# Kernel tuning notes

Hardware: AMD Instinct MI355X
Metric: run time of the kernel (lower is better)

## Reference

```python
import jax, jax.numpy as jnp
import numpy as np

N_NODES = 50000
N_EDGES = 600000
F_IN = 128   # nfeature
H = 128      # nhidden (must equal nfeature due to original code's gcn2 init)
C = 10       # nclass


def setup_inputs() -> dict:
    key = jax.random.key(0)
    ks = jax.random.split(key, 8)
    row = jax.random.randint(ks[0], (N_EDGES,), 0, N_NODES)
    col = jax.random.randint(ks[1], (N_EDGES,), 0, N_NODES)
    label = jax.random.randint(ks[2], (N_EDGES,), 0, C)
    features = jax.random.normal(ks[3], (N_NODES, F_IN), dtype=jnp.float32)
    s1 = 1.0 / np.sqrt(F_IN)
    W1 = jax.random.uniform(ks[4], (H, F_IN), jnp.float32, -s1, s1)
    b1 = jnp.zeros((H,), jnp.float32)
    s2 = 1.0 / np.sqrt(H)
    W2 = jax.random.uniform(ks[5], (H, H), jnp.float32, -s2, s2)
    b2 = jnp.zeros((H,), jnp.float32)
    s3 = 1.0 / np.sqrt(2 * H)
    Wfc = jax.random.uniform(ks[6], (C, 2 * H), jnp.float32, -s3, s3)
    bfc = jnp.zeros((C,), jnp.float32)
    return {"features": features, "W1": W1, "b1": b1, "W2": W2, "b2": b2,
            "Wfc": Wfc, "bfc": bfc, "row": row, "col": col, "label": label}


def gcn_conv(x, row, col, W, b):
    # GCNConv: add self loops, linear, then deg-normalized scatter-add.
    n = x.shape[0]
    sl = jnp.arange(n, dtype=row.dtype)
    r = jnp.concatenate([row, sl])  # source / j index (PyG edge_index[0])
    c = jnp.concatenate([col, sl])  # target / aggregation index (edge_index[1])
    h = x @ W.T + b  # [N, H]
    # degree computed over row of self-loop-augmented edge_index (>=1 always)
    deg = jax.ops.segment_sum(jnp.ones(r.shape, h.dtype), r, num_segments=n)
    dinv = deg ** -0.5
    norm = dinv[r] * dinv[c]  # [E+N]
    msg = norm[:, None] * h[r]  # gather + scale, [E+N, H]
    return jax.ops.segment_sum(msg, c, num_segments=n)  # scatter-add, [N, H]


def reference(features, W1, b1, W2, b2, Wfc, bfc, row, col, label):
    h1 = gcn_conv(features, row, col, W1, b1)  # [N, H]
    h2 = gcn_conv(h1, row, col, W2, b2)        # [N, H]
    # take_logits: index_select per edge endpoint, concat on feature dim
    x = jnp.concatenate([h2[row], h2[col]], axis=1)  # [E, 2H]
    logits = x @ Wfc.T + bfc  # [E, C]
    logp = jax.nn.log_softmax(logits, axis=-1)
    loss = -jnp.mean(jnp.take_along_axis(logp, label[:, None], axis=1))
    return loss, logits
```

## Files before the change

kernel.cpp:

```cpp
#include <hip/hip_runtime.h>
#include <hip/hip_bf16.h>
#include <math.h>

#define NND 50000
#define NE  600000
#define HD  128
#define NC  10
#define CAP 64
#define NCH 64
#define ECHUNK 9375
#define HBIN8 25000
#define SCB 128
#define HISTB 256
#define PREPB 1040
#define GEMMB 782
#define LOSSB 2344

typedef unsigned short ushort_t;
typedef unsigned char uchar_t;
typedef __attribute__((ext_vector_type(8))) short short8;
typedef __attribute__((ext_vector_type(4))) float f32x4;

__device__ __forceinline__ float bf2f(unsigned short u) {
  return __uint_as_float(((unsigned int)u) << 16);
}
__device__ __forceinline__ unsigned short f2bf(float f) {
  __hip_bfloat16 h = __float2bfloat16(f);
  return *(unsigned short*)&h;
}

__device__ __forceinline__ short8 f2bf8(const float* __restrict__ p) {
  float4 x0 = *(const float4*)p;
  float4 x1 = *(const float4*)(p + 4);
  short8 v;
  v[0] = (short)f2bf(x0.x); v[1] = (short)f2bf(x0.y);
  v[2] = (short)f2bf(x0.z); v[3] = (short)f2bf(x0.w);
  v[4] = (short)f2bf(x1.x); v[5] = (short)f2bf(x1.y);
  v[6] = (short)f2bf(x1.z); v[7] = (short)f2bf(x1.w);
  return v;
}

__global__ __launch_bounds__(256) void k_prep(const int* __restrict__ row,
                                              const int* __restrict__ col,
                                              uchar_t* __restrict__ partC,
                                              uchar_t* __restrict__ partR,
                                              const float* __restrict__ W1,
                                              const float* __restrict__ W2,
                                              const float* __restrict__ Wfc,
                                              const float* __restrict__ b1,
                                              const float* __restrict__ b2,
                                              float* __restrict__ M,
                                              float* __restrict__ uv) {
  __shared__ unsigned int h32[HBIN8 / 4];
  int bb = blockIdx.x, tid = threadIdx.x;
  if (bb < HISTB) {
    const int* src = (bb < SCB) ? col : row;
    uchar_t* dst = (bb < SCB) ? partC : partR;
    int hb = bb & (SCB - 1);
    int cb = hb & 63, half = hb >> 6;
    int binbase = half * HBIN8;
    for (int i = tid; i < HBIN8 / 4; i += 256) h32[i] = 0;
    __syncthreads();
    int e0 = cb * ECHUNK;
    for (int e = e0 + tid; e < e0 + ECHUNK; e += 256) {
      int r = src[e] - binbase;
      if (r >= 0 && r < HBIN8)
        atomicAdd(&h32[r >> 2], 1u << ((r & 3) * 8));
    }
    __syncthreads();
    unsigned int* d32 = (unsigned int*)(dst + (size_t)hb * HBIN8);
    for (int i = tid; i < HBIN8 / 4; i += 256) d32[i] = h32[i];
  } else {
    int wid = (bb - HISTB) * 4 + (tid >> 6);
    int lane = tid & 63;
    int c5 = wid / 130, jj = wid - c5 * 130;
    if (c5 >= 32) return;
    int grp = c5 >> 4, n = c5 & 15;
    bool valid = (n < NC);
    const float* wrow = &Wfc[(valid ? n : 0) * 256 + grp * 128];
    int k0 = lane, k1 = lane + 64;
    float v0 = 0.f, v1 = 0.f;
    for (int m = 0; m < 128; m++) {
      float wm = wrow[m];
      v0 += wm * W2[m * HD + k0];
      v1 += wm * W2[m * HD + k1];
    }
    float t;
    if (jj < 128)       t = v0 * W1[k0 * HD + jj] + v1 * W1[k1 * HD + jj];
    else if (jj == 128) t = v0 * b1[k0] + v1 * b1[k1];
    else                t = wrow[k0] * b2[k0] + wrow[k1] * b2[k1];
    if (!valid) t = 0.f;
    #pragma unroll
    for (int off = 32; off > 0; off >>= 1) t += __shfl_xor(t, off, 64);
    if (lane == 0) {
      if (jj < 128) M[(grp * 16 + n) * HD + jj] = t;
      else if (valid && jj == 128) uv[grp * 10 + n] = t;
      else if (valid) uv[20 + grp * 10 + n] = t;
    }
  }
}

__global__ __launch_bounds__(256) void k_off(const uchar_t* __restrict__ partC,
                                             const uchar_t* __restrict__ partR,
                                             uchar_t* __restrict__ off8,
                                             int* __restrict__ pos,
                                             float* __restrict__ dinv,
                                             float* __restrict__ out) {
  int n = blockIdx.x * 256 + threadIdx.x;
  if (n == 0) out[0] = 0.f;
  if (n >= NND) return;
  int half = (n >= HBIN8) ? 1 : 0;
  int local = n - half * HBIN8;
  int run = 0;
  #pragma unroll 8
  for (int cb = 0; cb < NCH; cb++) {
    int v = partC[(size_t)(half * NCH + cb) * HBIN8 + local];
    off8[(size_t)cb * NND + n] = (uchar_t)run;
    run += v;
  }
  pos[n] = run;
  int rs = 0;
  #pragma unroll 8
  for (int cb = 0; cb < NCH; cb++) rs += partR[(size_t)(half * NCH + cb) * HBIN8 + local];
  dinv[n] = rsqrtf(1.0f + (float)rs);
}

__global__ __launch_bounds__(256) void k_front(const int* __restrict__ row,
                                               const int* __restrict__ col,
                                               const uchar_t* __restrict__ off8,
                                               ushort_t* __restrict__ srcs,
                                               const float* __restrict__ features,
                                               const float* __restrict__ M,
                                               ushort_t* __restrict__ T0) {
  __shared__ unsigned int h32[HBIN8 / 4];
  int tid = threadIdx.x, bb = blockIdx.x;
  if (bb < SCB) {
    int cb = bb & 63, half = bb >> 6;
    int binbase = half * HBIN8;
    for (int i = tid; i < HBIN8 / 4; i += 256) h32[i] = 0;
    __syncthreads();
    int e0 = cb * ECHUNK;
    const uchar_t* offc = &off8[(size_t)cb * NND];
    for (int e = e0 + tid; e < e0 + ECHUNK; e += 256) {
      int c = col[e];
      int r = c - binbase;
      if (r >= 0 && r < HBIN8) {
        unsigned int old = atomicAdd(&h32[r >> 2], 1u << ((r & 3) * 8));
        int loc = (old >> ((r & 3) * 8)) & 0xff;
        int p = offc[c] + loc;
        if (p < CAP) srcs[(size_t)c * CAP + p] = (ushort_t)row[e];
      }
    }
  } else {
    int bid = bb - SCB;
    int w = tid >> 6, lane = tid & 63;
    int m = lane & 15, q = lane >> 4;
    short8 B[8];
    #pragma unroll
    for (int g = 0; g < 8; g++) {
      int grp = g >> 2, t = g & 3;
      B[g] = f2bf8(&M[(grp * 16 + m) * HD + t * 32 + q * 8]);
    }
    int rowbase = bid * 64 + w * 16;
    int rm = rowbase + m; if (rm >= NND) rm = NND - 1;
    short8 a[4];
    #pragma unroll
    for (int t = 0; t < 4; t++)
      a[t] = f2bf8(&features[(long)rm * HD + t * 32 + q * 8]);
    f32x4 accL = {0.f, 0.f, 0.f, 0.f}, accR = {0.f, 0.f, 0.f, 0.f};
    #pragma unroll
    for (int t = 0; t < 4; t++) {
      accL = __builtin_amdgcn_mfma_f32_16x16x32_bf16(a[t], B[t],     accL, 0, 0, 0);
      accR = __builtin_amdgcn_mfma_f32_16x16x32_bf16(a[t], B[4 + t], accR, 0, 0, 0);
    }
    if (m < 12) {
      #pragma unroll
      for (int reg = 0; reg < 4; reg++) {
        int r = rowbase + q * 4 + reg;
        if (r < NND) {
          float vL = (m < 10) ? accL[reg] : ((m == 10) ? 1.0f : 0.0f);
          float vR = (m < 10) ? accR[reg] : 0.0f;
          T0[(long)r * 24 + m]      = f2bf(vL);
          T0[(long)r * 24 + 12 + m] = f2bf(vR);
        }
      }
    }
  }
}

template <bool FINAL>
__global__ __launch_bounds__(256) void k_aggrn(const ushort_t* __restrict__ Q,
                                               const ushort_t* __restrict__ srcs,
                                               const int* __restrict__ pos,
                                               const float* __restrict__ dinv,
                                               ushort_t* __restrict__ T1,
                                               float* __restrict__ Pr,
                                               float* __restrict__ Pc,
                                               const float* __restrict__ uv) {
  int g = threadIdx.x >> 5, lane = threadIdx.x & 31;
  int half = lane >> 4;
  int f = lane & 15;
  int node = blockIdx.x * 8 + g;
  if (node >= NND) return;
  float di = dinv[node];
  bool act = (f < 12);
  unsigned int qv = act ? *(const unsigned int*)&Q[(long)node * 24 + 2 * f] : 0u;
  float sw = (half == 0) ? di * di : 0.f;
  float a0 = sw * bf2f((ushort_t)(qv & 0xffff));
  float a1 = sw * bf2f((ushort_t)(qv >> 16));
  int cnt = pos[node]; if (cnt > CAP) cnt = CAP;
  const ushort_t* nb = &srcs[(long)node * CAP];
  for (int base = 0; base < cnt; base += 32) {
    int m2 = cnt - base; if (m2 > 32) m2 = 32;
    int sl = 0; float wl = 0.f;
    if (lane < m2) { sl = (int)nb[base + lane]; wl = di * dinv[sl]; }
    int iters = (m2 + 1) >> 1;
    int u = 0;
    for (; u + 1 < iters; u += 2) {
      int t0 = 2 * u + half, t1 = t0 + 2;
      int s0 = __shfl(sl, t0 & 31, 32); float w0 = __shfl(wl, t0 & 31, 32);
      int s1 = __shfl(sl, t1 & 31, 32); float w1 = __shfl(wl, t1 & 31, 32);
      unsigned int h0 = act ? *(const unsigned int*)&Q[(long)s0 * 24 + 2 * f] : 0u;
      unsigned int h1 = act ? *(const unsigned int*)&Q[(long)s1 * 24 + 2 * f] : 0u;
      a0 += w0 * bf2f((ushort_t)(h0 & 0xffff));
      a1 += w0 * bf2f((ushort_t)(h0 >> 16));
      a0 += w1 * bf2f((ushort_t)(h1 & 0xffff));
      a1 += w1 * bf2f((ushort_t)(h1 >> 16));
    }
    if (u < iters) {
      int t = 2 * u + half;
      int s = __shfl(sl, t & 31, 32); float wv = __shfl(wl, t & 31, 32);
      unsigned int hs = act ? *(const unsigned int*)&Q[(long)s * 24 + 2 * f] : 0u;
      a0 += wv * bf2f((ushort_t)(hs & 0xffff));
      a1 += wv * bf2f((ushort_t)(hs >> 16));
    }
  }
  a0 += __shfl(a0, f + 16, 32);
  a1 += __shfl(a1, f + 16, 32);
  if (FINAL) {
    float s_i = __shfl(bf2f((ushort_t)(qv & 0xffff)), 5, 32);
    float z2  = __shfl(a0, 5, 32);
    if (half == 0) {
      if (f < 5) {
        int cc = 2 * f;
        float2 v;
        v.x = a0 + z2 * uv[cc]     + s_i * uv[20 + cc];
        v.y = a1 + z2 * uv[cc + 1] + s_i * uv[20 + cc + 1];
        *(float2*)&Pr[(long)node * 12 + cc] = v;
      } else if (f >= 6 && f < 11) {
        int cc = 2 * f - 12;
        float2 v;
        v.x = a0 + z2 * uv[10 + cc]     + s_i * uv[30 + cc];
        v.y = a1 + z2 * uv[10 + cc + 1] + s_i * uv[30 + cc + 1];
        *(float2*)&Pc[(long)node * 12 + cc] = v;
      }
    }
  } else {
    if (half == 0 && act) {
      unsigned int o = ((unsigned int)f2bf(a1) << 16) | (unsigned int)f2bf(a0);
      *(unsigned int*)&T1[(long)node * 24 + 2 * f] = o;
    }
  }
}

__global__ __launch_bounds__(256) void k_edge(const float* __restrict__ Pr,
                                              const float* __restrict__ Pc,
                                              const int* __restrict__ row,
                                              const int* __restrict__ col,
                                              const int* __restrict__ label,
                                              const float* __restrict__ bfc,
                                              float* __restrict__ logits,
                                              float* __restrict__ out) {
  __shared__ __align__(16) float S[2560];
  __shared__ float Ls[4];
  int tid = threadIdx.x;
  long e0 = (long)blockIdx.x * 256;
  int e = (int)e0 + tid;
  float lp = 0.f;
  if (e < NE) {
    int r = row[e], c = col[e];
    const float* pr = &Pr[(long)r * 12];
    const float* pc = &Pc[(long)c * 12];
    float4 r0 = *(const float4*)&pr[0];
    float4 r1 = *(const float4*)&pr[4];
    float4 r2 = *(const float4*)&pr[8];
    float4 c0 = *(const float4*)&pc[0];
    float4 c1 = *(const float4*)&pc[4];
    float4 c2 = *(const float4*)&pc[8];
    float p[NC];
    p[0] = r0.x + c0.x + bfc[0]; p[1] = r0.y + c0.y + bfc[1];
    p[2] = r0.z + c0.z + bfc[2]; p[3] = r0.w + c0.w + bfc[3];
    p[4] = r1.x + c1.x + bfc[4]; p[5] = r1.y + c1.y + bfc[5];
    p[6] = r1.z + c1.z + bfc[6]; p[7] = r1.w + c1.w + bfc[7];
    p[8] = r2.x + c2.x + bfc[8]; p[9] = r2.y + c2.y + bfc[9];
    #pragma unroll
    for (int cc = 0; cc < NC; cc++) S[tid * 10 + cc] = p[cc];
    float mx = p[0];
    #pragma unroll
    for (int cc = 1; cc < NC; cc++) mx = fmaxf(mx, p[cc]);
    float se = 0.f;
    #pragma unroll
    for (int cc = 0; cc < NC; cc++) se += __expf(p[cc] - mx);
    int lb = label[e];
    float plb = p[0];
    #pragma unroll
    for (int cc = 1; cc < NC; cc++) plb = (cc == lb) ? p[cc] : plb;
    lp = plb - mx - __logf(se);
  }
  __syncthreads();
  int ve = NE - (int)e0; if (ve > 256) ve = 256;
  int limF4 = ve * 10 / 4;
  float4* dst = (float4*)&logits[e0 * 10];
  const float4* src4 = (const float4*)S;
  for (int i = tid; i < limF4; i += 256) dst[i] = src4[i];
  #pragma unroll
  for (int off = 32; off > 0; off >>= 1) lp += __shfl_xor(lp, off, 64);
  if ((tid & 63) == 0) Ls[tid >> 6] = lp;
  __syncthreads();
  if (tid == 0)
    atomicAdd(out, -(Ls[0] + Ls[1] + Ls[2] + Ls[3]) / (float)NE);
}

extern "C" void kernel_launch(void* const* d_in, const int* in_sizes, int n_in,
                              void* d_out, int out_size, void* d_ws, size_t ws_size,
                              hipStream_t stream) {
  const float* features = (const float*)d_in[0];
  const float* W1  = (const float*)d_in[1];
  const float* b1  = (const float*)d_in[2];
  const float* W2  = (const float*)d_in[3];
  const float* b2  = (const float*)d_in[4];
  const float* Wfc = (const float*)d_in[5];
  const float* bfc = (const float*)d_in[6];
  const int* row   = (const int*)d_in[7];
  const int* col   = (const int*)d_in[8];
  const int* label = (const int*)d_in[9];
  float* out = (float*)d_out;

  float* ws = (float*)d_ws;
  size_t o = 0;
  int* pos = (int*)(ws + o);            o += 50048;
  float* dinv = ws + o;                 o += 50048;
  ushort_t* srcs = (ushort_t*)(ws + o); o += (size_t)NND * CAP / 2;
  uchar_t* partC = (uchar_t*)(ws + o);  o += SCB * HBIN8 / 4;
  uchar_t* partR = (uchar_t*)(ws + o);  o += SCB * HBIN8 / 4;
  uchar_t* off8  = (uchar_t*)(ws + o);  o += NCH * NND / 4;
  float* Pr = ws + o;                   o += 600000;
  float* Pc = ws + o;                   o += 600000;
  float* uv = ws + o;                   o += 64;
  float* M  = ws + o;                   o += 4096;
  ushort_t* T0 = (ushort_t*)(ws + o);   o += 600000;
  ushort_t* T1 = (ushort_t*)(ws + o);   o += 600000;

  k_prep<<<HISTB + PREPB, 256, 0, stream>>>(row, col, partC, partR,
                                            W1, W2, Wfc, b1, b2, M, uv);
  k_off<<<196, 256, 0, stream>>>(partC, partR, off8, pos, dinv, out);
  k_front<<<SCB + GEMMB, 256, 0, stream>>>(row, col, off8, srcs, features, M, T0);
  k_aggrn<false><<<6250, 256, 0, stream>>>(T0, srcs, pos, dinv, T1, nullptr, nullptr, uv);
  k_aggrn<true><<<6250, 256, 0, stream>>>(T1, srcs, pos, dinv, nullptr, Pr, Pc, uv);
  k_edge<<<LOSSB, 256, 0, stream>>>(Pr, Pc, row, col, label, bfc, out + 1, out);
}
```

Before: 219.6 us.

## Fuse offset computation into histogram kernel via global atomics, drop k_off

Removes the separate offset/degree kernel. Histogram blocks now atomically add their per-chunk bin counts into global pos/deg arrays and store the returned base as the 8-bit offset. The Wfc·W2·W1 precompute is restructured to one block per output row using shared memory, with fewer blocks. Degree normalization is computed on the fly with rsqrt in the aggregation kernels, and a memset is added to zero the counters. This saves one launch and the partial-histogram round trip, but offsets now depend on atomic ordering across chunks rather than chunk order, and many global atomics are added.

Result: slower. 267.1 us (+21.6%).

```diff
diff --git a/kernel.cpp b/kernel.cpp
--- a/kernel.cpp
+++ b/kernel.cpp
@@ -12,7 +12,7 @@
 #define HBIN8 25000
 #define SCB 128
 #define HISTB 256
-#define PREPB 1040
+#define COLB 32
 #define GEMMB 782
 #define LOSSB 2344
 
@@ -42,20 +42,22 @@
 
 __global__ __launch_bounds__(256) void k_prep(const int* __restrict__ row,
                                               const int* __restrict__ col,
-                                              uchar_t* __restrict__ partC,
-                                              uchar_t* __restrict__ partR,
+                                              int* __restrict__ pos,
+                                              int* __restrict__ deg,
+                                              uchar_t* __restrict__ off8,
                                               const float* __restrict__ W1,
                                               const float* __restrict__ W2,
                                               const float* __restrict__ Wfc,
                                               const float* __restrict__ b1,
                                               const float* __restrict__ b2,
                                               float* __restrict__ M,
-                                              float* __restrict__ uv) {
-  __shared__ unsigned int h32[HBIN8 / 4];
+                                              float* __restrict__ uv,
+                                              float* __restrict__ out) {
   int bb = blockIdx.x, tid = threadIdx.x;
   if (bb < HISTB) {
-    const int* src = (bb < SCB) ? col : row;
-    uchar_t* dst = (bb < SCB) ? partC : partR;
+    __shared__ unsigned int h32[HBIN8 / 4];
+    bool isCol = (bb < SCB);
+    const int* src = isCol ? col : row;
     int hb = bb & (SCB - 1);
     int cb = hb & 63, half = hb >> 6;
     int binbase = half * HBIN8;
@@ -68,61 +70,59 @@
         atomicAdd(&h32[r >> 2], 1u << ((r & 3) * 8));
     }
     __syncthreads();
-    unsigned int* d32 = (unsigned int*)(dst + (size_t)hb * HBIN8);
-    for (int i = tid; i < HBIN8 / 4; i += 256) d32[i] = h32[i];
+    if (isCol) {
+      unsigned int* d32 = (unsigned int*)(off8 + (size_t)cb * NND + binbase);
+      int* pb = pos + binbase;
+      for (int i = tid; i < HBIN8 / 4; i += 256) {
+        unsigned int cv = h32[i], ov = 0;
+        #pragma unroll
+        for (int j = 0; j < 4; j++) {
+          int cnt = (cv >> (8 * j)) & 0xff;
+          if (cnt) {
+            int b = atomicAdd(&pb[4 * i + j], cnt);
+            ov |= ((unsigned int)(b & 0xff)) << (8 * j);
+          }
+        }
+        d32[i] = ov;
+      }
+    } else {
+      int* pb = deg + binbase;
+      for (int i = tid; i < HBIN8 / 4; i += 256) {
+        unsigned int cv = h32[i];
+        #pragma unroll
+        for (int j = 0; j < 4; j++) {
+          int cnt = (cv >> (8 * j)) & 0xff;
+          if (cnt) atomicAdd(&pb[4 * i + j], cnt);
+        }
+      }
+    }
   } else {
-    int wid = (bb - HISTB) * 4 + (tid >> 6);
-    int lane = tid & 63;
-    int c5 = wid / 130, jj = wid - c5 * 130;
-    if (c5 >= 32) return;
+    __shared__ float V[128];
+    int c5 = bb - HISTB;
+    if (c5 == 0 && tid == 0) out[0] = 0.f;
     int grp = c5 >> 4, n = c5 & 15;
     bool valid = (n < NC);
     const float* wrow = &Wfc[(valid ? n : 0) * 256 + grp * 128];
-    int k0 = lane, k1 = lane + 64;
-    float v0 = 0.f, v1 = 0.f;
-    for (int m = 0; m < 128; m++) {
-      float wm = wrow[m];
-      v0 += wm * W2[m * HD + k0];
-      v1 += wm * W2[m * HD + k1];
-    }
-    float t;
-    if (jj < 128)       t = v0 * W1[k0 * HD + jj] + v1 * W1[k1 * HD + jj];
-    else if (jj == 128) t = v0 * b1[k0] + v1 * b1[k1];
-    else                t = wrow[k0] * b2[k0] + wrow[k1] * b2[k1];
-    if (!valid) t = 0.f;
-    #pragma unroll
-    for (int off = 32; off > 0; off >>= 1) t += __shfl_xor(t, off, 64);
-    if (lane == 0) {
-      if (jj < 128) M[(grp * 16 + n) * HD + jj] = t;
-      else if (valid && jj == 128) uv[grp * 10 + n] = t;
-      else if (valid) uv[20 + grp * 10 + n] = t;
-    }
-  }
-}
-
-__global__ __launch_bounds__(256) void k_off(const uchar_t* __restrict__ partC,
-                                             const uchar_t* __restrict__ partR,
-                                             uchar_t* __restrict__ off8,
-                                             int* __restrict__ pos,
-                                             float* __restrict__ dinv,
-                                             float* __restrict__ out) {
-  int n = blockIdx.x * 256 + threadIdx.x;
-  if (n == 0) out[0] = 0.f;
-  if (n >= NND) return;
-  int half = (n >= HBIN8) ? 1 : 0;
-  int local = n - half * HBIN8;
-  int run = 0;
-  #pragma unroll 8
-  for (int cb = 0; cb < NCH; cb++) {
-    int v = partC[(size_t)(half * NCH + cb) * HBIN8 + local];
-    off8[(size_t)cb * NND + n] = (uchar_t)run;
-    run += v;
-  }
-  pos[n] = run;
-  int rs = 0;
-  #pragma unroll 8
-  for (int cb = 0; cb < NCH; cb++) rs += partR[(size_t)(half * NCH + cb) * HBIN8 + local];
-  dinv[n] = rsqrtf(1.0f + (float)rs);
+    if (tid < 128) {
+      float s = 0.f;
+      for (int m = 0; m < 128; m++) s += wrow[m] * W2[m * HD + tid];
+      V[tid] = s;
+    }
+    __syncthreads();
+    if (tid < 128) {
+      float t = 0.f;
+      for (int k = 0; k < 128; k++) t += V[k] * W1[k * HD + tid];
+      M[(grp * 16 + n) * HD + tid] = valid ? t : 0.f;
+    } else if (tid == 128 && valid) {
+      float t = 0.f;
+      for (int k = 0; k < 128; k++) t += V[k] * b1[k];
+      uv[grp * 10 + n] = t;
+    } else if (tid == 129 && valid) {
+      float t = 0.f;
+      for (int k = 0; k < 128; k++) t += wrow[k] * b2[k];
+      uv[20 + grp * 10 + n] = t;
+    }
+  }
 }
 
 __global__ __launch_bounds__(256) void k_front(const int* __restrict__ row,
@@ -192,7 +192,7 @@
 __global__ __launch_bounds__(256) void k_aggrn(const ushort_t* __restrict__ Q,
                                                const ushort_t* __restrict__ srcs,
                                                const int* __restrict__ pos,
-                                               const float* __restrict__ dinv,
+                                               const int* __restrict__ deg,
                                                ushort_t* __restrict__ T1,
                                                float* __restrict__ Pr,
                                                float* __restrict__ Pc,
@@ -202,7 +202,7 @@
   int f = lane & 15;
   int node = blockIdx.x * 8 + g;
   if (node >= NND) return;
-  float di = dinv[node];
+  float di = rsqrtf(1.0f + (float)deg[node]);
   bool act = (f < 12);
   unsigned int qv = act ? *(const unsigned int*)&Q[(long)node * 24 + 2 * f] : 0u;
   float sw = (half == 0) ? di * di : 0.f;
@@ -213,7 +213,7 @@
   for (int base = 0; base < cnt; base += 32) {
     int m2 = cnt - base; if (m2 > 32) m2 = 32;
     int sl = 0; float wl = 0.f;
-    if (lane < m2) { sl = (int)nb[base + lane]; wl = di * dinv[sl]; }
+    if (lane < m2) { sl = (int)nb[base + lane]; wl = di * rsqrtf(1.0f + (float)deg[sl]); }
     int iters = (m2 + 1) >> 1;
     int u = 0;
     for (; u + 1 < iters; u += 2) {
@@ -339,10 +339,8 @@
   float* ws = (float*)d_ws;
   size_t o = 0;
   int* pos = (int*)(ws + o);            o += 50048;
-  float* dinv = ws + o;                 o += 50048;
+  int* deg = (int*)(ws + o);            o += 50048;
   ushort_t* srcs = (ushort_t*)(ws + o); o += (size_t)NND * CAP / 2;
-  uchar_t* partC = (uchar_t*)(ws + o);  o += SCB * HBIN8 / 4;
-  uchar_t* partR = (uchar_t*)(ws + o);  o += SCB * HBIN8 / 4;
   uchar_t* off8  = (uchar_t*)(ws + o);  o += NCH * NND / 4;
   float* Pr = ws + o;                   o += 600000;
   float* Pc = ws + o;                   o += 600000;
@@ -351,11 +349,11 @@
   ushort_t* T0 = (ushort_t*)(ws + o);   o += 600000;
   ushort_t* T1 = (ushort_t*)(ws + o);   o += 600000;
 
-  k_prep<<<HISTB + PREPB, 256, 0, stream>>>(row, col, partC, partR,
-                                            W1, W2, Wfc, b1, b2, M, uv);
-  k_off<<<196, 256, 0, stream>>>(partC, partR, off8, pos, dinv, out);
+  hipMemsetAsync(pos, 0, 2 * 50048 * sizeof(int), stream);
+  k_prep<<<HISTB + COLB, 256, 0, stream>>>(row, col, pos, deg, off8,
+                                           W1, W2, Wfc, b1, b2, M, uv, out);
   k_front<<<SCB + GEMMB, 256, 0, stream>>>(row, col, off8, srcs, features, M, T0);
-  k_aggrn<false><<<6250, 256, 0, stream>>>(T0, srcs, pos, dinv, T1, nullptr, nullptr, uv);
-  k_aggrn<true><<<6250, 256, 0, stream>>>(T1, srcs, pos, dinv, nullptr, Pr, Pc, uv);
+  k_aggrn<false><<<6250, 256, 0, stream>>>(T0, srcs, pos, deg, T1, nullptr, nullptr, uv);
+  k_aggrn<true><<<6250, 256, 0, stream>>>(T1, srcs, pos, deg, nullptr, Pr, Pc, uv);
   k_edge<<<LOSSB, 256, 0, stream>>>(Pr, Pc, row, col, label, bfc, out + 1, out);
 }
```
